# Kernel tuning notes

Hardware: AMD Instinct MI355X
Metric: run time of the kernel (lower is better)

## Reference

```python
import jax, jax.numpy as jnp
import numpy as np


def setup_inputs() -> dict:
    key = jax.random.key(0)
    k1, k2 = jax.random.split(key)
    B, N, D = 4, 2048, 1024
    x = jax.random.normal(k1, (B, N, D), dtype=jnp.float32)
    # torch nn.Linear weight shape [out_features, in_features] = [3D, D]
    w_qkv = jax.random.normal(k2, (3 * D, D), dtype=jnp.float32) * (D ** -0.5)
    return {"x": x, "w_qkv": w_qkv}


def reference(x, w_qkv):
    D = x.shape[-1]
    scale = D ** -0.5
    qkv = jnp.einsum('bnd,ed->bne', x, w_qkv)  # [B, N, 3D]
    q, k, v = jnp.split(qkv, 3, axis=-1)
    scores = jnp.einsum('bnd,bmd->bnm', q, k) * scale  # [B, N, N]
    attn = jax.nn.softmax(scores, axis=-1)
    return jnp.einsum('bnm,bmd->bnd', attn, v)
```

## Files before the change

### kernel.cpp

```cpp
#include <hip/hip_runtime.h>
#include <hip/hip_bf16.h>


typedef __bf16 bf16x8 __attribute__((ext_vector_type(8)));
typedef float f32x4 __attribute__((ext_vector_type(4)));

__device__ __forceinline__ void store_out(float* p, float v) { *p = v; }
__device__ __forceinline__ void store_out(__hip_bfloat16* p, float v) { *p = __float2bfloat16(v); }

#define MFMA16(a, b, c) __builtin_amdgcn_mfma_f32_16x16x32_bf16(a, b, c, 0, 0, 0)

__global__ __launch_bounds__(256)
void cast_f32_bf16(const float* __restrict__ in, __hip_bfloat16* __restrict__ out, int n4) {
  for (int i = blockIdx.x * blockDim.x + threadIdx.x; i < n4; i += gridDim.x * blockDim.x) {
    float4 v = ((const float4*)in)[i];
    __hip_bfloat16 b0 = __float2bfloat16(v.x), b1 = __float2bfloat16(v.y),
                   b2 = __float2bfloat16(v.z), b3 = __float2bfloat16(v.w);
    ushort4 o;
    o.x = *(unsigned short*)&b0; o.y = *(unsigned short*)&b1;
    o.z = *(unsigned short*)&b2; o.w = *(unsigned short*)&b3;
    ((ushort4*)out)[i] = o;
  }
}


#define PHASE(P, CB, PF, K0N)                                                          \
  {                                                                                    \
    bf16x8 af[MFRAGS][2];                                                              \
    _Pragma("unroll") for (int mf = 0; mf < MFRAGS; ++mf) {                            \
      af[mf][0] = frag(CB, 0, wm * (MFRAGS * 64) + (P * MFRAGS + mf) * 16, 0);         \
      af[mf][1] = frag(CB, 0, wm * (MFRAGS * 64) + (P * MFRAGS + mf) * 16, 1);         \
    }                                                                                  \
    if (P == 0) {                                                                      \
      _Pragma("unroll") for (int j = 0; j < 4; ++j) {                                  \
        bfr[j][0] = frag(CB, 1, wn * 64 + j * 16, 0);                                  \
        bfr[j][1] = frag(CB, 1, wn * 64 + j * 16, 1);                                  \
      }                                                                                \
      if (PF) stage_all(CB ^ 1, K0N);                                                  \
      asm volatile("s_waitcnt lgkmcnt(8)" ::: "memory");                               \
    }                                                                                  \
    __builtin_amdgcn_s_barrier();                                                      \
    asm volatile("s_waitcnt lgkmcnt(0)" ::: "memory");                                 \
    __builtin_amdgcn_sched_barrier(0);                                                 \
    __builtin_amdgcn_s_setprio(1);                                                     \
    _Pragma("unroll") for (int j = 0; j < 4; ++j)                                      \
      _Pragma("unroll") for (int mf = 0; mf < MFRAGS; ++mf) {                          \
        acc[P * MFRAGS + mf][j] = MFMA16(af[mf][0], bfr[j][0], acc[P * MFRAGS + mf][j]); \
        acc[P * MFRAGS + mf][j] = MFMA16(af[mf][1], bfr[j][1], acc[P * MFRAGS + mf][j]); \
      }                                                                                \
    __builtin_amdgcn_s_setprio(0);                                                     \
    if (P == 3) asm volatile("s_waitcnt vmcnt(0)" ::: "memory");                       \
    __builtin_amdgcn_s_barrier();                                                      \
  }

template <typename OutT, int MFRAGS>
__global__ __launch_bounds__(512, 2)
void gemm256(const __hip_bfloat16* __restrict__ A, int lda, long sA,
             const __hip_bfloat16* __restrict__ B, int ldb, long sB,
             OutT* __restrict__ C, int ldc, long sC,
             int K, float cscale) {
  constexpr int BM = MFRAGS * 128;
  constexpr int ABYTES = BM * 64 * 2;
  constexpr int BUFSZ = ABYTES + 32768;
  extern __shared__ char smem[];
  const int tid = threadIdx.x, lane = tid & 63, wid = tid >> 6;
  const int wm = wid >> 2, wn = wid & 3;
  A += (long)blockIdx.z * sA; B += (long)blockIdx.z * sB; C += (long)blockIdx.z * sC;
  const long bm = (long)blockIdx.x * BM, bn = (long)blockIdx.y * 256;
  const int laneOff = (lane & 15) * 64 + (((lane >> 4) * 16) ^ ((lane & 8) ? 32 : 0));
  const int sRowA = (wid >> 1) * 16 + (lane >> 2);
  const int sKs = wid & 1;
  const int sCol = ((lane & 3) * 8) ^ ((lane & 32) ? 16 : 0);
  const int nt = K >> 6;

  auto stage = [&](int cbuf, int reg , int row0, int k0) {
    const __hip_bfloat16* g =
        reg ? (B + (bn + row0 + sRowA) * (long)ldb + k0 + sKs * 32 + sCol)
            : (A + (bm + row0 + sRowA) * (long)lda + k0 + sKs * 32 + sCol);
    char* dst = smem + cbuf * BUFSZ + (reg ? ABYTES : 0) + ((row0 >> 4) * 2 + wid) * 1024;
    __builtin_amdgcn_global_load_lds((const __attribute__((address_space(1))) void*)g,
                                     (__attribute__((address_space(3))) void*)dst, 16, 0, 0);
  };
  auto stage_all = [&](int cbuf, int k0) {
    stage(cbuf, 0, 0, k0); stage(cbuf, 0, 64, k0);
    if (MFRAGS == 2) { stage(cbuf, 0, 128, k0); stage(cbuf, 0, 192, k0); }
    stage(cbuf, 1, 0, k0); stage(cbuf, 1, 64, k0);
    stage(cbuf, 1, 128, k0); stage(cbuf, 1, 192, k0);
  };
  auto frag = [&](int cbuf, int reg, int R, int ks) -> bf16x8 {
    return *(const bf16x8*)(smem + cbuf * BUFSZ + (reg ? ABYTES : 0) +
                            ((R >> 4) * 2 + ks) * 1024 + laneOff);
  };

  f32x4 acc[MFRAGS * 4][4] = {};
  bf16x8 bfr[4][2];

  stage_all(0, 0);
  asm volatile("s_waitcnt vmcnt(0)" ::: "memory");
  __builtin_amdgcn_s_barrier();

  for (int t = 0; t < nt; t += 2) {
    {
      const int k0n = (t + 1) << 6;
      PHASE(0, 0, true, k0n) PHASE(1, 0, true, k0n)
      PHASE(2, 0, true, k0n) PHASE(3, 0, true, k0n)
    }
    {
      const bool pf = (t + 2) < nt;
      const int k0n = (t + 2) << 6;
      PHASE(0, 1, pf, k0n) PHASE(1, 1, pf, k0n)
      PHASE(2, 1, pf, k0n) PHASE(3, 1, pf, k0n)
    }
  }

  const int r0 = (lane >> 4) * 4, cn = lane & 15;
#pragma unroll
  for (int rf = 0; rf < MFRAGS * 4; ++rf)
#pragma unroll
    for (int j = 0; j < 4; ++j) {
      long row = bm + wm * (MFRAGS * 64) + rf * 16 + r0;
      long col = bn + wn * 64 + j * 16 + cn;
#pragma unroll
      for (int jj = 0; jj < 4; ++jj)
        store_out(&C[(row + jj) * (long)ldc + col], acc[rf][j][jj] * cscale);
    }
}

__global__ __launch_bounds__(256)
void transpose_v(const __hip_bfloat16* __restrict__ qkv, __hip_bfloat16* __restrict__ Vt) {
  __shared__ __hip_bfloat16 tile[32][33];
  const int b = blockIdx.z;
  const __hip_bfloat16* V = qkv + (size_t)b * 2048 * 3072 + 2048;
  __hip_bfloat16* vt = Vt + (size_t)b * 1024 * 2048;
  const int tx = threadIdx.x & 31, ty = threadIdx.x >> 5;
  const int m0 = blockIdx.x * 32, d0 = blockIdx.y * 32;
#pragma unroll
  for (int i = 0; i < 32; i += 8)
    tile[ty + i][tx] = V[(size_t)(m0 + ty + i) * 3072 + d0 + tx];
  __syncthreads();
#pragma unroll
  for (int i = 0; i < 32; i += 8)
    vt[(size_t)(d0 + ty + i) * 2048 + m0 + tx] = tile[tx][ty + i];
}

__global__ __launch_bounds__(256)
void softmax_rows(float* __restrict__ S) {
  float* row = S + (size_t)blockIdx.x * 2048;
  const int t = threadIdx.x, lane = t & 63, wid = t >> 6;
  float4 v0 = ((const float4*)row)[t];
  float4 v1 = ((const float4*)row)[256 + t];
  float vals[8] = {v0.x, v0.y, v0.z, v0.w, v1.x, v1.y, v1.z, v1.w};
  float m = vals[0];
#pragma unroll
  for (int i = 1; i < 8; ++i) m = fmaxf(m, vals[i]);
#pragma unroll
  for (int o = 32; o; o >>= 1) m = fmaxf(m, __shfl_xor(m, o));
  __shared__ float red[4];
  if (lane == 0) red[wid] = m;
  __syncthreads();
  m = fmaxf(fmaxf(red[0], red[1]), fmaxf(red[2], red[3]));
  __syncthreads();
  float p[8], s = 0.f;
#pragma unroll
  for (int i = 0; i < 8; ++i) { p[i] = __expf(vals[i] - m); s += p[i]; }
#pragma unroll
  for (int o = 32; o; o >>= 1) s += __shfl_xor(s, o);
  if (lane == 0) red[wid] = s;
  __syncthreads();
  s = red[0] + red[1] + red[2] + red[3];
  const float inv = 1.0f / s;
  __hip_bfloat16 b[8];
#pragma unroll
  for (int i = 0; i < 8; ++i) b[i] = __float2bfloat16(p[i] * inv);
  ushort4 o0, o1;
  o0.x = *(unsigned short*)&b[0]; o0.y = *(unsigned short*)&b[1];
  o0.z = *(unsigned short*)&b[2]; o0.w = *(unsigned short*)&b[3];
  o1.x = *(unsigned short*)&b[4]; o1.y = *(unsigned short*)&b[5];
  o1.z = *(unsigned short*)&b[6]; o1.w = *(unsigned short*)&b[7];
  unsigned short* prow = (unsigned short*)row;
  ((ushort4*)prow)[t] = o0;
  ((ushort4*)prow)[256 + t] = o1;
}

extern "C" void kernel_launch(void* const* d_in, const int* in_sizes, int n_in,
                              void* d_out, int out_size, void* d_ws, size_t ws_size,
                              hipStream_t stream) {
  const float* x = (const float*)d_in[0];
  const float* w = (const float*)d_in[1];
  float* out = (float*)d_out;
  char* ws = (char*)d_ws;

  __hip_bfloat16* xb  = (__hip_bfloat16*)ws;
  __hip_bfloat16* wb  = (__hip_bfloat16*)(ws + 16777216);
  float*          S   = (float*)ws;
  __hip_bfloat16* qkv = (__hip_bfloat16*)(ws + 67108864);
  __hip_bfloat16* Vt  = (__hip_bfloat16*)(ws + 117440512);

  cast_f32_bf16<<<1024, 256, 0, stream>>>(x, xb, (4 * 2048 * 1024) / 4);
  cast_f32_bf16<<<512, 256, 0, stream>>>(w, wb, (3072 * 1024) / 4);

  gemm256<__hip_bfloat16, 2><<<dim3(32, 12, 1), 512, 131072, stream>>>(
      xb, 1024, 0L, wb, 1024, 0L, qkv, 3072, 0L, 1024, 1.0f);

  transpose_v<<<dim3(64, 32, 4), 256, 0, stream>>>(qkv, Vt);

  gemm256<float, 2><<<dim3(8, 8, 4), 512, 131072, stream>>>(
      qkv, 3072, (long)2048 * 3072, qkv + 1024, 3072, (long)2048 * 3072,
      S, 2048, (long)2048 * 2048, 1024, 0.03125f);

  softmax_rows<<<8192, 256, 0, stream>>>(S);

  gemm256<float, 1><<<dim3(16, 4, 4), 512, 98304, stream>>>(
      (const __hip_bfloat16*)S, 4096, (long)2048 * 4096,
      Vt, 2048, (long)1024 * 2048,
      out, 1024, (long)2048 * 1024, 2048, 1.0f);
}
```

Baseline: 260.9 us.

## Spread GEMM tile prefetch across phases with fine-grained vmcnt waits; vectorize V transpose

The GEMM main loop no longer issues the whole next-tile prefetch at phase 0 followed by a full vmcnt(0) drain. Global-to-LDS loads are now split into pairs spread across the four MFMA phases, B tiles are staged further ahead, and partial vmcnt waits replace the full drain, with an explicit epilogue for the last two k-tiles. The aim is to keep memory traffic overlapped with MFMA work and cut barrier stalls. The V transpose also moves to 64x64 tiles with ushort4 vector loads and stores. The hand-tuned wait counts are fragile: a wrong count would be a data race.

```diff
diff --git a/kernel.cpp b/kernel.cpp
--- a/kernel.cpp
+++ b/kernel.cpp
@@ -9,6 +9,8 @@
 __device__ __forceinline__ void store_out(__hip_bfloat16* p, float v) { *p = __float2bfloat16(v); }
 
 #define MFMA16(a, b, c) __builtin_amdgcn_mfma_f32_16x16x32_bf16(a, b, c, 0, 0, 0)
+#define VMW(n) asm volatile("s_waitcnt vmcnt(" #n ")" ::: "memory")
+#define NOSTAGE ((void)0)
 
 __global__ __launch_bounds__(256)
 void cast_f32_bf16(const float* __restrict__ in, __hip_bfloat16* __restrict__ out, int n4) {
@@ -24,32 +26,31 @@
 }
 
 
-#define PHASE(P, CB, PF, K0N)                                                          \
+#define PHASE(P, CB, STAGES, WAITC)                                                    \
   {                                                                                    \
     bf16x8 af[MFRAGS][2];                                                              \
     _Pragma("unroll") for (int mf = 0; mf < MFRAGS; ++mf) {                            \
-      af[mf][0] = frag(CB, 0, wm * (MFRAGS * 64) + (P * MFRAGS + mf) * 16, 0);         \
-      af[mf][1] = frag(CB, 0, wm * (MFRAGS * 64) + (P * MFRAGS + mf) * 16, 1);         \
+      af[mf][0] = frag(CB, 0, wm * (MFRAGS * 64) + ((P) * MFRAGS + mf) * 16, 0);       \
+      af[mf][1] = frag(CB, 0, wm * (MFRAGS * 64) + ((P) * MFRAGS + mf) * 16, 1);       \
     }                                                                                  \
-    if (P == 0) {                                                                      \
+    if ((P) == 0) {                                                                    \
       _Pragma("unroll") for (int j = 0; j < 4; ++j) {                                  \
         bfr[j][0] = frag(CB, 1, wn * 64 + j * 16, 0);                                  \
         bfr[j][1] = frag(CB, 1, wn * 64 + j * 16, 1);                                  \
       }                                                                                \
-      if (PF) stage_all(CB ^ 1, K0N);                                                  \
-      asm volatile("s_waitcnt lgkmcnt(8)" ::: "memory");                               \
     }                                                                                  \
+    STAGES;                                                                            \
     __builtin_amdgcn_s_barrier();                                                      \
     asm volatile("s_waitcnt lgkmcnt(0)" ::: "memory");                                 \
     __builtin_amdgcn_sched_barrier(0);                                                 \
     __builtin_amdgcn_s_setprio(1);                                                     \
     _Pragma("unroll") for (int j = 0; j < 4; ++j)                                      \
       _Pragma("unroll") for (int mf = 0; mf < MFRAGS; ++mf) {                          \
-        acc[P * MFRAGS + mf][j] = MFMA16(af[mf][0], bfr[j][0], acc[P * MFRAGS + mf][j]); \
-        acc[P * MFRAGS + mf][j] = MFMA16(af[mf][1], bfr[j][1], acc[P * MFRAGS + mf][j]); \
+        acc[(P) * MFRAGS + mf][j] = MFMA16(af[mf][0], bfr[j][0], acc[(P) * MFRAGS + mf][j]); \
+        acc[(P) * MFRAGS + mf][j] = MFMA16(af[mf][1], bfr[j][1], acc[(P) * MFRAGS + mf][j]); \
       }                                                                                \
     __builtin_amdgcn_s_setprio(0);                                                     \
-    if (P == 3) asm volatile("s_waitcnt vmcnt(0)" ::: "memory");                       \
+    WAITC;                                                                             \
     __builtin_amdgcn_s_barrier();                                                      \
   }
 
@@ -81,12 +82,6 @@
     __builtin_amdgcn_global_load_lds((const __attribute__((address_space(1))) void*)g,
                                      (__attribute__((address_space(3))) void*)dst, 16, 0, 0);
   };
-  auto stage_all = [&](int cbuf, int k0) {
-    stage(cbuf, 0, 0, k0); stage(cbuf, 0, 64, k0);
-    if (MFRAGS == 2) { stage(cbuf, 0, 128, k0); stage(cbuf, 0, 192, k0); }
-    stage(cbuf, 1, 0, k0); stage(cbuf, 1, 64, k0);
-    stage(cbuf, 1, 128, k0); stage(cbuf, 1, 192, k0);
-  };
   auto frag = [&](int cbuf, int reg, int R, int ks) -> bf16x8 {
     return *(const bf16x8*)(smem + cbuf * BUFSZ + (reg ? ABYTES : 0) +
                             ((R >> 4) * 2 + ks) * 1024 + laneOff);
@@ -95,21 +90,67 @@
   f32x4 acc[MFRAGS * 4][4] = {};
   bf16x8 bfr[4][2];
 
-  stage_all(0, 0);
-  asm volatile("s_waitcnt vmcnt(0)" ::: "memory");
-  __builtin_amdgcn_s_barrier();
-
-  for (int t = 0; t < nt; t += 2) {
+  if constexpr (MFRAGS == 2) {
+    stage(0, 1, 0, 0); stage(0, 1, 64, 0); stage(0, 1, 128, 0); stage(0, 1, 192, 0);
+    stage(0, 0, 0, 0); stage(0, 0, 128, 0);
+    stage(0, 0, 64, 0); stage(0, 0, 192, 0);
+    stage(1, 1, 0, 64); stage(1, 1, 64, 64); stage(1, 1, 128, 64); stage(1, 1, 192, 64);
+    stage(1, 0, 0, 64); stage(1, 0, 128, 64);
+    VMW(8);
+    __builtin_amdgcn_s_barrier();
+
+    for (int t = 0; t < nt - 2; t += 2) {
+      const int ka = (t + 1) << 6, kb = (t + 2) << 6;
+      PHASE(0, 0, (stage(1, 0, 64, ka), stage(1, 0, 192, ka)), NOSTAGE)
+      PHASE(1, 0, (stage(0, 1, 0, kb), stage(0, 1, 64, kb)), VMW(10))
+      PHASE(2, 0, (stage(0, 1, 128, kb), stage(0, 1, 192, kb)), NOSTAGE)
+      PHASE(3, 0, (stage(0, 0, 0, kb), stage(0, 0, 128, kb)), VMW(8))
+      const int kc = (t + 2) << 6, kd = (t + 3) << 6;
+      PHASE(0, 1, (stage(0, 0, 64, kc), stage(0, 0, 192, kc)), NOSTAGE)
+      PHASE(1, 1, (stage(1, 1, 0, kd), stage(1, 1, 64, kd)), VMW(10))
+      PHASE(2, 1, (stage(1, 1, 128, kd), stage(1, 1, 192, kd)), NOSTAGE)
+      PHASE(3, 1, (stage(1, 0, 0, kd), stage(1, 0, 128, kd)), VMW(8))
+    }
     {
-      const int k0n = (t + 1) << 6;
-      PHASE(0, 0, true, k0n) PHASE(1, 0, true, k0n)
-      PHASE(2, 0, true, k0n) PHASE(3, 0, true, k0n)
+      const int ke = (nt - 1) << 6;
+      PHASE(0, 0, (stage(1, 0, 64, ke), stage(1, 0, 192, ke)), NOSTAGE)
+      PHASE(1, 0, NOSTAGE, VMW(8))
+      PHASE(2, 0, NOSTAGE, NOSTAGE)
+      PHASE(3, 0, NOSTAGE, VMW(2))
+      PHASE(0, 1, NOSTAGE, NOSTAGE)
+      PHASE(1, 1, NOSTAGE, VMW(0))
+      PHASE(2, 1, NOSTAGE, NOSTAGE)
+      PHASE(3, 1, NOSTAGE, NOSTAGE)
+    }
+  } else {
+    stage(0, 1, 0, 0); stage(0, 1, 64, 0); stage(0, 1, 128, 0); stage(0, 1, 192, 0);
+    stage(0, 0, 0, 0); stage(0, 0, 64, 0);
+    stage(1, 1, 0, 64); stage(1, 1, 64, 64); stage(1, 1, 128, 64); stage(1, 1, 192, 64);
+    VMW(4);
+    __builtin_amdgcn_s_barrier();
+
+    for (int t = 0; t < nt - 2; t += 2) {
+      const int ka = (t + 1) << 6, kb = (t + 2) << 6;
+      PHASE(0, 0, (stage(1, 0, 0, ka), stage(1, 0, 64, ka)), NOSTAGE)
+      PHASE(1, 0, (stage(0, 1, 0, kb), stage(0, 1, 64, kb)), NOSTAGE)
+      PHASE(2, 0, (stage(0, 1, 128, kb), stage(0, 1, 192, kb)), NOSTAGE)
+      PHASE(3, 0, NOSTAGE, VMW(4))
+      const int kc = (t + 2) << 6, kd = (t + 3) << 6;
+      PHASE(0, 1, (stage(0, 0, 0, kc), stage(0, 0, 64, kc)), NOSTAGE)
+      PHASE(1, 1, (stage(1, 1, 0, kd), stage(1, 1, 64, kd)), NOSTAGE)
+      PHASE(2, 1, (stage(1, 1, 128, kd), stage(1, 1, 192, kd)), NOSTAGE)
+      PHASE(3, 1, NOSTAGE, VMW(4))
     }
     {
-      const bool pf = (t + 2) < nt;
-      const int k0n = (t + 2) << 6;
-      PHASE(0, 1, pf, k0n) PHASE(1, 1, pf, k0n)
-      PHASE(2, 1, pf, k0n) PHASE(3, 1, pf, k0n)
+      const int ke = (nt - 1) << 6;
+      PHASE(0, 0, (stage(1, 0, 0, ke), stage(1, 0, 64, ke)), NOSTAGE)
+      PHASE(1, 0, NOSTAGE, NOSTAGE)
+      PHASE(2, 0, NOSTAGE, NOSTAGE)
+      PHASE(3, 0, NOSTAGE, VMW(0))
+      PHASE(0, 1, NOSTAGE, NOSTAGE)
+      PHASE(1, 1, NOSTAGE, NOSTAGE)
+      PHASE(2, 1, NOSTAGE, NOSTAGE)
+      PHASE(3, 1, NOSTAGE, NOSTAGE)
     }
   }
 
@@ -128,19 +169,28 @@
 
 __global__ __launch_bounds__(256)
 void transpose_v(const __hip_bfloat16* __restrict__ qkv, __hip_bfloat16* __restrict__ Vt) {
-  __shared__ __hip_bfloat16 tile[32][33];
+  __shared__ unsigned short tr[64][68];
   const int b = blockIdx.z;
-  const __hip_bfloat16* V = qkv + (size_t)b * 2048 * 3072 + 2048;
-  __hip_bfloat16* vt = Vt + (size_t)b * 1024 * 2048;
-  const int tx = threadIdx.x & 31, ty = threadIdx.x >> 5;
-  const int m0 = blockIdx.x * 32, d0 = blockIdx.y * 32;
-#pragma unroll
-  for (int i = 0; i < 32; i += 8)
-    tile[ty + i][tx] = V[(size_t)(m0 + ty + i) * 3072 + d0 + tx];
-  __syncthreads();
-#pragma unroll
-  for (int i = 0; i < 32; i += 8)
-    vt[(size_t)(d0 + ty + i) * 2048 + m0 + tx] = tile[tx][ty + i];
+  const unsigned short* V = (const unsigned short*)(qkv + (size_t)b * 2048 * 3072 + 2048);
+  unsigned short* vt = (unsigned short*)(Vt + (size_t)b * 1024 * 2048);
+  const int m0 = blockIdx.x * 64, d0 = blockIdx.y * 64;
+  const int t = threadIdx.x;
+#pragma unroll
+  for (int i = 0; i < 4; ++i) {
+    int idx = i * 256 + t;
+    int m = idx >> 4, dc = (idx & 15) * 4;
+    ushort4 v = *(const ushort4*)&V[(size_t)(m0 + m) * 3072 + d0 + dc];
+    tr[dc + 0][m] = v.x; tr[dc + 1][m] = v.y; tr[dc + 2][m] = v.z; tr[dc + 3][m] = v.w;
+  }
+  __syncthreads();
+#pragma unroll
+  for (int i = 0; i < 4; ++i) {
+    int idx = i * 256 + t;
+    int d = idx >> 4, mc = (idx & 15) * 4;
+    ushort4 o;
+    o.x = tr[d][mc]; o.y = tr[d][mc + 1]; o.z = tr[d][mc + 2]; o.w = tr[d][mc + 3];
+    *(ushort4*)&vt[(size_t)(d0 + d) * 2048 + m0 + mc] = o;
+  }
 }
 
 __global__ __launch_bounds__(256)
@@ -202,7 +252,7 @@
   gemm256<__hip_bfloat16, 2><<<dim3(32, 12, 1), 512, 131072, stream>>>(
       xb, 1024, 0L, wb, 1024, 0L, qkv, 3072, 0L, 1024, 1.0f);
 
-  transpose_v<<<dim3(64, 32, 4), 256, 0, stream>>>(qkv, Vt);
+  transpose_v<<<dim3(32, 16, 4), 256, 0, stream>>>(qkv, Vt);
 
   gemm256<float, 2><<<dim3(8, 8, 4), 512, 131072, stream>>>(
       qkv, 3072, (long)2048 * 3072, qkv + 1024, 3072, (long)2048 * 3072,
```

New measurement: 247.1 us. 5.3% less time.
